# Optimization experiments

Measured on AMD Instinct MI355X. Metric: run time of the kernel, lower is better.

## Reference

```python
import jax, jax.numpy as jnp
import numpy as np
import math

H = 8
E = 512
D_K = E // H
NEG = -1000000000.0
# last (and only surviving) row of dist_bar: one threshold per head
DIST_BAR = np.array([0.2, 0.3, 0.4, 0.5, 0.6, 0.7, 0.8, 0.9], dtype=np.float32)


def setup_inputs() -> dict:
    key = jax.random.key(0)
    ks = jax.random.split(key, 12)
    B, N = 8, 1024
    s = 1.0 / math.sqrt(E)
    inp = {
        "query": jax.random.normal(ks[0], (B, N, E), jnp.float32),
        "key": jax.random.normal(ks[1], (B, N, E), jnp.float32),
        "value": jax.random.normal(ks[2], (B, N, E), jnp.float32),
        "dist": jax.random.uniform(ks[3], (B, 1, N, N), jnp.float32),
        "mask": jnp.ones((B, N, N), jnp.int32),
        "Wq": jax.random.normal(ks[4], (E, E), jnp.float32) * s,
        "bq": jnp.zeros((E,), jnp.float32),
        "Wk": jax.random.normal(ks[5], (E, E), jnp.float32) * s,
        "bk": jnp.zeros((E,), jnp.float32),
        "Wv": jax.random.normal(ks[6], (E, E), jnp.float32) * s,
        "bv": jnp.zeros((E,), jnp.float32),
        "Wo": jax.random.normal(ks[7], (E, E), jnp.float32) * s,
        "bo": jnp.zeros((E,), jnp.float32),
    }
    return inp


def reference(query, key, value, dist, mask, Wq, bq, Wk, bk, Wv, bv, Wo, bo):
    B, N, _ = query.shape
    # project and split heads: [B, H, N, D_K]
    def heads(x, W, b):
        return (x @ W.T + b).reshape(B, N, H, D_K).transpose(0, 2, 1, 3)
    q = heads(query, Wq, bq)
    k = heads(key, Wk, bk)
    v = heads(value, Wv, bv)
    scores = jnp.einsum("bhqd,bhkd->bhqk", q, k) / math.sqrt(D_K)
    # padding mask: [B,N,N] -> [B,1,N,N]
    scores = jnp.where(mask[:, None, :, :] == 0, NEG, scores)
    # per-head distance mask: dist [B,1,N,N] < thr[h] -> [B,H,N,N]
    thr = jnp.asarray(DIST_BAR)[None, :, None, None]
    dmask = dist < thr
    # first row/col (global atom) always attend
    dmask = dmask.at[:, :, 0, :].set(True).at[:, :, :, 0].set(True)
    scores = jnp.where(dmask, scores, NEG)
    p = jax.nn.softmax(scores, axis=-1)
    out = jnp.einsum("bhqk,bhkd->bhqd", p, v)  # [B,H,N,D_K]
    out = out.transpose(0, 2, 1, 3).reshape(B, N, H * D_K)
    return out @ Wo.T + bo
```

## Files before the change

kernel.cpp:

```cpp
#include <hip/hip_runtime.h>
#include <stdint.h>


typedef __attribute__((ext_vector_type(8))) short short8;
typedef __attribute__((ext_vector_type(4))) float floatx4;

#define MFMA16(a, b, c) __builtin_amdgcn_mfma_f32_16x16x32_bf16((a), (b), (c), 0, 0, 0)

static __device__ __forceinline__ unsigned short f2bf(float f) {
  union { float f; unsigned u; } v; v.f = f;
  unsigned r = v.u + 0x7fffu + ((v.u >> 16) & 1u);
  return (unsigned short)(r >> 16);
}

static __device__ __forceinline__ void gload_lds16(const void* g, void* l) {
  __builtin_amdgcn_global_load_lds((const __attribute__((address_space(1))) unsigned int*)g,
                                   (__attribute__((address_space(3))) unsigned int*)l,
                                   16, 0, 0);
}
static __device__ __forceinline__ int xsw(int row) { return (row & 3) ^ ((row >> 2) & 3); }

__global__ void wcast_kernel(const float* __restrict__ Wq, const float* __restrict__ Wk,
                             const float* __restrict__ Wv, const float* __restrict__ Wo,
                             unsigned short* __restrict__ o0, unsigned short* __restrict__ o1,
                             unsigned short* __restrict__ o2, unsigned short* __restrict__ o3) {
  int i = blockIdx.x * blockDim.x + threadIdx.x;
  int w = i >> 16, loc = i & 65535;
  const float* s = (w == 0) ? Wq : (w == 1) ? Wk : (w == 2) ? Wv : Wo;
  unsigned short* d = (w == 0) ? o0 : (w == 1) ? o1 : (w == 2) ? o2 : o3;
  float4 v = ((const float4*)s)[loc];
  ushort4 o;
  o.x = f2bf(v.x); o.y = f2bf(v.y); o.z = f2bf(v.z); o.w = f2bf(v.w);
  ((ushort4*)d)[loc] = o;
}

__global__ void codes_kernel(const float* __restrict__ dist, const int* __restrict__ mask,
                             unsigned char* __restrict__ codesP) {
  int t = blockIdx.x * blockDim.x + threadIdx.x;
  int flat = t << 2;
  int b = flat >> 20;
  int rem = flat & ((1 << 20) - 1);
  int row = rem >> 10;
  int col0 = rem & 1023;
  float4 d4 = ((const float4*)dist)[t];
  int4 m4 = ((const int4*)mask)[t];
  float dv[4] = {d4.x, d4.y, d4.z, d4.w};
  int mv[4] = {m4.x, m4.y, m4.z, m4.w};
  int rg = row >> 5;
  int st = (row >> 4) & 1;
  int qq = (row >> 2) & 3;
  int r = row & 3;
  size_t rowbase = (size_t)(b * 32 + rg) * 32768;
  int sub = st * 32 + r;
#pragma unroll
  for (int u = 0; u < 4; u++) {
    int col = col0 + u;
    float d = dv[u];
    int hmin = (d >= 0.2f) + (d >= 0.3f) + (d >= 0.4f) + (d >= 0.5f) +
               (d >= 0.6f) + (d >= 0.7f) + (d >= 0.8f) + (d >= 0.9f);
    unsigned char cc = (unsigned char)hmin;
    if (row == 0 || col == 0) cc = 0;
    if (mv[u] == 0) cc = 9;
    int kt = col >> 7, ci = (col >> 4) & 7, c = col & 15;
    int lane = qq * 16 + c;
    codesP[rowbase + (size_t)kt * 4096 + lane * 64 + sub + ci * 4] = cc;
  }
}

__global__ __launch_bounds__(256) void qkv_gemm(
    const float* __restrict__ Aq, const float* __restrict__ Ak, const float* __restrict__ Av,
    const unsigned short* __restrict__ Wqp, const unsigned short* __restrict__ Wkp,
    const unsigned short* __restrict__ Wvp,
    const float* __restrict__ bq, const float* __restrict__ bk, const float* __restrict__ bv,
    unsigned short* __restrict__ Qh, unsigned short* __restrict__ Kh,
    unsigned short* __restrict__ Vt) {
  const int z = blockIdx.z;
  const float* A = (z == 0) ? Aq : (z == 1) ? Ak : Av;
  const unsigned short* W = (z == 0) ? Wqp : (z == 1) ? Wkp : Wvp;
  const float* bias = (z == 0) ? bq : (z == 1) ? bk : bv;
  unsigned short* O = (z == 0) ? Qh : (z == 1) ? Kh : Vt;

  __shared__ __align__(16) short As[64 * 40];
  __shared__ __align__(16) short Bs[128 * 32];
  const int tid = threadIdx.x;
  const int lane = tid & 63;
  const int wave = tid >> 6;
  const int c = lane & 15;
  const int q = lane >> 4;
  const int m0 = blockIdx.x * 64;
  const int n0 = blockIdx.y * 128;
  const int wr = (wave >> 1) * 32;
  const int wc = (wave & 1) * 64;

  floatx4 acc[2][4];
#pragma unroll
  for (int i = 0; i < 2; i++)
#pragma unroll
    for (int j = 0; j < 4; j++) acc[i][j] = (floatx4)(0.0f);

  const int arow = tid >> 2, ach = tid & 3;
  const float* Ab = A + (size_t)(m0 + arow) * 512 + ach * 8;

  for (int k0 = 0; k0 < 512; k0 += 32) {
    __syncthreads();
#pragma unroll
    for (int it = 0; it < 2; it++) {
      int slot = wave * 128 + it * 64 + lane;
      int brow = slot >> 2, bch = slot & 3;
      int g = bch ^ xsw(brow);
      gload_lds16(W + (size_t)(n0 + brow) * 512 + k0 + g * 8,
                  &Bs[(size_t)(wave * 128 + it * 64) * 8]);
    }
    float4 a0 = *(const float4*)(Ab + k0);
    float4 a1 = *(const float4*)(Ab + k0 + 4);
    short8 av;
    av[0] = (short)f2bf(a0.x); av[1] = (short)f2bf(a0.y);
    av[2] = (short)f2bf(a0.z); av[3] = (short)f2bf(a0.w);
    av[4] = (short)f2bf(a1.x); av[5] = (short)f2bf(a1.y);
    av[6] = (short)f2bf(a1.z); av[7] = (short)f2bf(a1.w);
    *(short8*)(&As[arow * 40 + ach * 8]) = av;
    __syncthreads();

    short8 af[2], bfv[4];
#pragma unroll
    for (int i = 0; i < 2; i++)
      af[i] = *(const short8*)(&As[(wr + i * 16 + c) * 40 + q * 8]);
#pragma unroll
    for (int j = 0; j < 4; j++) {
      int row = wc + j * 16 + c;
      bfv[j] = *(const short8*)(&Bs[row * 32 + (q ^ xsw(row)) * 8]);
    }
#pragma unroll
    for (int i = 0; i < 2; i++)
#pragma unroll
      for (int j = 0; j < 4; j++)
        acc[i][j] = MFMA16(af[i], bfv[j], acc[i][j]);
  }

#pragma unroll
  for (int i = 0; i < 2; i++) {
    int gm0 = m0 + wr + i * 16 + q * 4;
#pragma unroll
    for (int j = 0; j < 4; j++) {
      int gn = n0 + wc + j * 16 + c;
      float bb = bias[gn];
      int h = gn >> 6, d = gn & 63;
      if (z == 2) {
        int b = gm0 >> 10, n = gm0 & 1023;
        ushort4 pk;
#pragma unroll
        for (int r = 0; r < 4; r++) pk[r] = f2bf(acc[i][j][r] + bb);
        *(ushort4*)(&Vt[(((size_t)(b * 8 + h) * 64 + d) << 10) + n]) = pk;
      } else {
#pragma unroll
        for (int r = 0; r < 4; r++) {
          int m = gm0 + r;
          int b = m >> 10, n = m & 1023;
          O[((((size_t)(b * 8 + h)) << 10) + n) * 64 + d] = f2bf(acc[i][j][r] + bb);
        }
      }
    }
  }
}

__global__ __launch_bounds__(256) void out_gemm(const unsigned short* __restrict__ A,
                                                const unsigned short* __restrict__ W,
                                                const float* __restrict__ bias,
                                                float* __restrict__ Out) {
  __shared__ __align__(16) short As[64 * 32];
  __shared__ __align__(16) short Bs[128 * 32];
  const int tid = threadIdx.x;
  const int lane = tid & 63;
  const int wave = tid >> 6;
  const int c = lane & 15;
  const int q = lane >> 4;
  const int m0 = blockIdx.x * 64;
  const int n0 = blockIdx.y * 128;
  const int wr = (wave >> 1) * 32;
  const int wc = (wave & 1) * 64;

  floatx4 acc[2][4];
#pragma unroll
  for (int i = 0; i < 2; i++)
#pragma unroll
    for (int j = 0; j < 4; j++) acc[i][j] = (floatx4)(0.0f);

  for (int k0 = 0; k0 < 512; k0 += 32) {
    __syncthreads();
    {
      int slot = wave * 64 + lane;
      int arow = slot >> 2, ach = slot & 3;
      int g = ach ^ xsw(arow);
      gload_lds16(A + (size_t)(m0 + arow) * 512 + k0 + g * 8, &As[(size_t)(wave * 64) * 8]);
    }
#pragma unroll
    for (int it = 0; it < 2; it++) {
      int slot = wave * 128 + it * 64 + lane;
      int brow = slot >> 2, bch = slot & 3;
      int g = bch ^ xsw(brow);
      gload_lds16(W + (size_t)(n0 + brow) * 512 + k0 + g * 8,
                  &Bs[(size_t)(wave * 128 + it * 64) * 8]);
    }
    __syncthreads();

    short8 af[2], bfv[4];
#pragma unroll
    for (int i = 0; i < 2; i++) {
      int row = wr + i * 16 + c;
      af[i] = *(const short8*)(&As[row * 32 + (q ^ xsw(row)) * 8]);
    }
#pragma unroll
    for (int j = 0; j < 4; j++) {
      int row = wc + j * 16 + c;
      bfv[j] = *(const short8*)(&Bs[row * 32 + (q ^ xsw(row)) * 8]);
    }
#pragma unroll
    for (int i = 0; i < 2; i++)
#pragma unroll
      for (int j = 0; j < 4; j++)
        acc[i][j] = MFMA16(af[i], bfv[j], acc[i][j]);
  }

#pragma unroll
  for (int i = 0; i < 2; i++) {
    int gm0 = m0 + wr + i * 16 + q * 4;
#pragma unroll
    for (int j = 0; j < 4; j++) {
      int gn = n0 + wc + j * 16 + c;
      float bb = bias[gn];
#pragma unroll
      for (int r = 0; r < 4; r++)
        Out[(size_t)(gm0 + r) * 512 + gn] = acc[i][j][r] + bb;
    }
  }
}

__global__ __launch_bounds__(256) void attn_kernel(const unsigned short* __restrict__ Qh,
                                                   const unsigned short* __restrict__ Kh,
                                                   const unsigned short* __restrict__ Vt,
                                                   const unsigned char* __restrict__ codesP,
                                                   unsigned short* __restrict__ AO) {
  __shared__ __align__(16) unsigned short P[4][32 * 132];
  const int tid = threadIdx.x;
  const int lane = tid & 63;
  const int wave = tid >> 6;
  const int wsub = wave & 1;
  const int whalf = wave >> 1;
  const int c = lane & 15;
  const int q = lane >> 4;
  const int bh = blockIdx.y;
  const int b = bh >> 3;
  const int h = bh & 7;
  const size_t base = (size_t)bh << 16;
  const int rbase = blockIdx.x * 64 + wsub * 32;
  const int rg = rbase >> 5;
  unsigned short* Pw = &P[wave][0];

  short8 aq[2][2];
#pragma unroll
  for (int st = 0; st < 2; st++)
#pragma unroll
    for (int kk = 0; kk < 2; kk++)
      aq[st][kk] = *(const short8*)(Qh + base + (size_t)(rbase + st * 16 + c) * 64 + kk * 32 + q * 8);

  const unsigned char* cbt = codesP + (size_t)(b * 32 + rg) * 32768 + lane * 64;
  const unsigned short* Kb = Kh + base;
  const unsigned short* Vb = Vt + base;

  float rs[2][4];
#pragma unroll
  for (int st = 0; st < 2; st++)
#pragma unroll
    for (int r = 0; r < 4; r++) rs[st][r] = 0.0f;
  floatx4 o[2][4];
#pragma unroll
  for (int st = 0; st < 2; st++)
#pragma unroll
    for (int ci = 0; ci < 4; ci++) o[st][ci] = (floatx4)(0.0f);

  for (int kti = 0; kti < 4; kti++) {
    const int kt = whalf * 4 + kti;
    const unsigned short* Kt = Kb + (size_t)kt * 128 * 64;
    floatx4 s[2][8];
#pragma unroll
    for (int ci = 0; ci < 8; ci++) { s[0][ci] = (floatx4)(0.0f); s[1][ci] = (floatx4)(0.0f); }
#pragma unroll
    for (int ci = 0; ci < 8; ci++)
#pragma unroll
      for (int kk = 0; kk < 2; kk++) {
        short8 bk = *(const short8*)(Kt + (size_t)(ci * 16 + c) * 64 + kk * 32 + q * 8);
        s[0][ci] = MFMA16(aq[0][kk], bk, s[0][ci]);
        s[1][ci] = MFMA16(aq[1][kk], bk, s[1][ci]);
      }
    const unsigned char* cp = cbt + (size_t)kt * 4096;
    uint4 w0 = *(const uint4*)(cp);
    uint4 w1 = *(const uint4*)(cp + 16);
    uint4 w2 = *(const uint4*)(cp + 32);
    uint4 w3 = *(const uint4*)(cp + 48);
    unsigned cv[16] = {w0.x, w0.y, w0.z, w0.w, w1.x, w1.y, w1.z, w1.w,
                       w2.x, w2.y, w2.z, w2.w, w3.x, w3.y, w3.z, w3.w};
#pragma unroll
    for (int st = 0; st < 2; st++)
#pragma unroll
      for (int ci = 0; ci < 8; ci++)
#pragma unroll
        for (int r = 0; r < 4; r++) {
          int bidx = st * 32 + ci * 4 + r;
          int code = (cv[bidx >> 2] >> ((bidx & 3) * 8)) & 0xff;
          float e = (h >= code) ? exp2f(s[st][ci][r] * 0.1803368801111362f) : 0.0f;
          rs[st][r] += e;
          Pw[(st * 16 + q * 4 + r) * 132 + ci * 16 + c] = f2bf(e);
        }
#pragma unroll
    for (int ch = 0; ch < 4; ch++) {
      short8 ap0 = *(const short8*)(&Pw[(size_t)c * 132 + ch * 32 + q * 8]);
      short8 ap1 = *(const short8*)(&Pw[(size_t)(16 + c) * 132 + ch * 32 + q * 8]);
#pragma unroll
      for (int ci = 0; ci < 4; ci++) {
        short8 bv = *(const short8*)(Vb + (size_t)(ci * 16 + c) * 1024 + kt * 128 + ch * 32 + q * 8);
        o[0][ci] = MFMA16(ap0, bv, o[0][ci]);
        o[1][ci] = MFMA16(ap1, bv, o[1][ci]);
      }
    }
  }

  float* Pf = (float*)&P[0][0];
  __syncthreads();
  if (whalf == 1) {
#pragma unroll
    for (int st = 0; st < 2; st++)
#pragma unroll
      for (int ci = 0; ci < 4; ci++)
        *(floatx4*)&Pf[(((wsub * 10 + st * 4 + ci) * 64) + lane) * 4] = o[st][ci];
#pragma unroll
    for (int st = 0; st < 2; st++) {
      floatx4 rr;
#pragma unroll
      for (int r = 0; r < 4; r++) rr[r] = rs[st][r];
      *(floatx4*)&Pf[(((wsub * 10 + 8 + st) * 64) + lane) * 4] = rr;
    }
  }
  __syncthreads();
  if (whalf == 1) return;

#pragma unroll
  for (int st = 0; st < 2; st++)
#pragma unroll
    for (int ci = 0; ci < 4; ci++) {
      floatx4 p = *(const floatx4*)&Pf[(((wsub * 10 + st * 4 + ci) * 64) + lane) * 4];
      o[st][ci] += p;
    }
#pragma unroll
  for (int st = 0; st < 2; st++) {
    floatx4 pr = *(const floatx4*)&Pf[(((wsub * 10 + 8 + st) * 64) + lane) * 4];
#pragma unroll
    for (int r = 0; r < 4; r++) rs[st][r] += pr[r];
  }

  float inv[2][4];
#pragma unroll
  for (int st = 0; st < 2; st++)
#pragma unroll
    for (int r = 0; r < 4; r++) {
      float v = rs[st][r];
      v += __shfl_xor(v, 1); v += __shfl_xor(v, 2);
      v += __shfl_xor(v, 4); v += __shfl_xor(v, 8);
      inv[st][r] = 1.0f / v;
    }
#pragma unroll
  for (int st = 0; st < 2; st++)
#pragma unroll
    for (int r = 0; r < 4; r++) {
      int n = rbase + st * 16 + q * 4 + r;
      size_t ob = ((size_t)((b << 10) + n)) * 512 + h * 64;
#pragma unroll
      for (int ci = 0; ci < 4; ci++)
        AO[ob + ci * 16 + c] = f2bf(o[st][ci][r] * inv[st][r]);
    }
}

extern "C" void kernel_launch(void* const* d_in, const int* in_sizes, int n_in,
                              void* d_out, int out_size, void* d_ws, size_t ws_size,
                              hipStream_t stream) {
  const float* query = (const float*)d_in[0];
  const float* key_  = (const float*)d_in[1];
  const float* value = (const float*)d_in[2];
  const float* dist  = (const float*)d_in[3];
  const int*   mask  = (const int*)d_in[4];
  const float* Wq = (const float*)d_in[5];
  const float* bq = (const float*)d_in[6];
  const float* Wk = (const float*)d_in[7];
  const float* bk = (const float*)d_in[8];
  const float* Wv = (const float*)d_in[9];
  const float* bv = (const float*)d_in[10];
  const float* Wo = (const float*)d_in[11];
  const float* bo = (const float*)d_in[12];

  char* ws = (char*)d_ws;
  size_t off = 0;
  auto alloc = [&](size_t bytes) -> char* {
    char* p = ws + off;
    off += (bytes + 255) & ~(size_t)255;
    return p;
  };
  const size_t NQKV = 8192ull * 512;
  unsigned short* wq16 = (unsigned short*)alloc(512ull * 512 * 2);
  unsigned short* wk16 = (unsigned short*)alloc(512ull * 512 * 2);
  unsigned short* wv16 = (unsigned short*)alloc(512ull * 512 * 2);
  unsigned short* wo16 = (unsigned short*)alloc(512ull * 512 * 2);
  unsigned short* Qh = (unsigned short*)alloc(NQKV * 2);
  unsigned short* Kh = (unsigned short*)alloc(NQKV * 2);
  unsigned short* Vt = (unsigned short*)alloc(NQKV * 2);
  unsigned short* AO = (unsigned short*)alloc(NQKV * 2);
  unsigned char*  codesP = (unsigned char*)alloc(8ull * 1024 * 1024);

  wcast_kernel<<<1024, 256, 0, stream>>>(Wq, Wk, Wv, Wo, wq16, wk16, wv16, wo16);
  codes_kernel<<<8192, 256, 0, stream>>>(dist, mask, codesP);
  qkv_gemm<<<dim3(128, 4, 3), 256, 0, stream>>>(query, key_, value, wq16, wk16, wv16,
                                                bq, bk, bv, Qh, Kh, Vt);
  attn_kernel<<<dim3(16, 64), 256, 0, stream>>>(Qh, Kh, Vt, codesP, AO);
  out_gemm<<<dim3(128, 4), 256, 0, stream>>>(AO, wo16, bo, (float*)d_out);
}
```

Measured before the change: 308.3 us.

## Chunk attention QK/softmax/PV into 32-key slices to cut register pressure

The per-128-key tile is split into four 32-key chunks, each computing scores, masking/exp, writing P to LDS, and immediately doing the PV MFMAs. The full 2x8 score accumulator array is no longer live at once, and the codes are loaded per chunk instead of 64 bytes up front. Launch bounds now request 3 blocks per CU to push register use down. A sched_barrier per chunk restricts compiler interleaving across chunks, which may reduce latency hiding.

```diff
diff --git a/kernel.cpp b/kernel.cpp
--- a/kernel.cpp
+++ b/kernel.cpp
@@ -235,11 +235,11 @@
   }
 }
 
-__global__ __launch_bounds__(256) void attn_kernel(const unsigned short* __restrict__ Qh,
-                                                   const unsigned short* __restrict__ Kh,
-                                                   const unsigned short* __restrict__ Vt,
-                                                   const unsigned char* __restrict__ codesP,
-                                                   unsigned short* __restrict__ AO) {
+__global__ __launch_bounds__(256, 3) void attn_kernel(const unsigned short* __restrict__ Qh,
+                                                      const unsigned short* __restrict__ Kh,
+                                                      const unsigned short* __restrict__ Vt,
+                                                      const unsigned char* __restrict__ codesP,
+                                                      unsigned short* __restrict__ AO) {
   __shared__ __align__(16) unsigned short P[4][32 * 132];
   const int tid = threadIdx.x;
   const int lane = tid & 63;
@@ -281,46 +281,50 @@
   for (int kti = 0; kti < 4; kti++) {
     const int kt = whalf * 4 + kti;
     const unsigned short* Kt = Kb + (size_t)kt * 128 * 64;
-    floatx4 s[2][8];
-#pragma unroll
-    for (int ci = 0; ci < 8; ci++) { s[0][ci] = (floatx4)(0.0f); s[1][ci] = (floatx4)(0.0f); }
-#pragma unroll
-    for (int ci = 0; ci < 8; ci++)
-#pragma unroll
-      for (int kk = 0; kk < 2; kk++) {
-        short8 bk = *(const short8*)(Kt + (size_t)(ci * 16 + c) * 64 + kk * 32 + q * 8);
-        s[0][ci] = MFMA16(aq[0][kk], bk, s[0][ci]);
-        s[1][ci] = MFMA16(aq[1][kk], bk, s[1][ci]);
+    const unsigned char* cp = cbt + (size_t)kt * 4096;
+#pragma unroll
+    for (int j = 0; j < 4; j++) {
+      floatx4 s[2][2];
+      s[0][0] = (floatx4)(0.0f); s[0][1] = (floatx4)(0.0f);
+      s[1][0] = (floatx4)(0.0f); s[1][1] = (floatx4)(0.0f);
+#pragma unroll
+      for (int u = 0; u < 2; u++) {
+        int ci = 2 * j + u;
+#pragma unroll
+        for (int kk = 0; kk < 2; kk++) {
+          short8 bk = *(const short8*)(Kt + (size_t)(ci * 16 + c) * 64 + kk * 32 + q * 8);
+          s[0][u] = MFMA16(aq[0][kk], bk, s[0][u]);
+          s[1][u] = MFMA16(aq[1][kk], bk, s[1][u]);
+        }
       }
-    const unsigned char* cp = cbt + (size_t)kt * 4096;
-    uint4 w0 = *(const uint4*)(cp);
-    uint4 w1 = *(const uint4*)(cp + 16);
-    uint4 w2 = *(const uint4*)(cp + 32);
-    uint4 w3 = *(const uint4*)(cp + 48);
-    unsigned cv[16] = {w0.x, w0.y, w0.z, w0.w, w1.x, w1.y, w1.z, w1.w,
-                       w2.x, w2.y, w2.z, w2.w, w3.x, w3.y, w3.z, w3.w};
-#pragma unroll
-    for (int st = 0; st < 2; st++)
-#pragma unroll
-      for (int ci = 0; ci < 8; ci++)
-#pragma unroll
-        for (int r = 0; r < 4; r++) {
-          int bidx = st * 32 + ci * 4 + r;
-          int code = (cv[bidx >> 2] >> ((bidx & 3) * 8)) & 0xff;
-          float e = (h >= code) ? exp2f(s[st][ci][r] * 0.1803368801111362f) : 0.0f;
-          rs[st][r] += e;
-          Pw[(st * 16 + q * 4 + r) * 132 + ci * 16 + c] = f2bf(e);
+      uint2 cw0 = *(const uint2*)(cp + j * 8);
+      uint2 cw1 = *(const uint2*)(cp + 32 + j * 8);
+#pragma unroll
+      for (int st = 0; st < 2; st++) {
+        unsigned we = st ? cw1.x : cw0.x;
+        unsigned wo = st ? cw1.y : cw0.y;
+#pragma unroll
+        for (int u = 0; u < 2; u++) {
+          unsigned wv = u ? wo : we;
+          int ci = 2 * j + u;
+#pragma unroll
+          for (int r = 0; r < 4; r++) {
+            int code = (wv >> (r * 8)) & 0xff;
+            float e = (h >= code) ? exp2f(s[st][u][r] * 0.1803368801111362f) : 0.0f;
+            rs[st][r] += e;
+            Pw[(st * 16 + q * 4 + r) * 132 + ci * 16 + c] = f2bf(e);
+          }
         }
-#pragma unroll
-    for (int ch = 0; ch < 4; ch++) {
-      short8 ap0 = *(const short8*)(&Pw[(size_t)c * 132 + ch * 32 + q * 8]);
-      short8 ap1 = *(const short8*)(&Pw[(size_t)(16 + c) * 132 + ch * 32 + q * 8]);
-#pragma unroll
-      for (int ci = 0; ci < 4; ci++) {
-        short8 bv = *(const short8*)(Vb + (size_t)(ci * 16 + c) * 1024 + kt * 128 + ch * 32 + q * 8);
-        o[0][ci] = MFMA16(ap0, bv, o[0][ci]);
-        o[1][ci] = MFMA16(ap1, bv, o[1][ci]);
       }
+      short8 ap0 = *(const short8*)(&Pw[(size_t)c * 132 + j * 32 + q * 8]);
+      short8 ap1 = *(const short8*)(&Pw[(size_t)(16 + c) * 132 + j * 32 + q * 8]);
+#pragma unroll
+      for (int co = 0; co < 4; co++) {
+        short8 bv = *(const short8*)(Vb + (size_t)(co * 16 + c) * 1024 + kt * 128 + j * 32 + q * 8);
+        o[0][co] = MFMA16(ap0, bv, o[0][co]);
+        o[1][co] = MFMA16(ap1, bv, o[1][co]);
+      }
+      __builtin_amdgcn_sched_barrier(0);
     }
   }
 
```

After: 290.5 us. -5.8%, faster.
